# Kernel optimization log

Measured on AMD Instinct MI355X. Metric: run time of the kernel, lower is better.

Reference implementation:

```python
import jax, jax.numpy as jnp
import numpy as np

K = 16          # patch_size
P2 = 256        # patch_size**2
D_PD = 512      # learned base dictionary atoms (D_out_lam_pd)
D_LAM = 112     # adaptive atoms from sdict, = 8*14 (D_out_lam)
DD = D_PD + D_LAM  # 624
T = 5
INDICE = 112
MIN_V, MAX_V = 0.0, 1.0


def _idx(H, W, k, stride):
    oh = (H - k) // stride + 1
    ow = (W - k) // stride + 1
    r = jnp.arange(k)[:, None] + stride * jnp.arange(oh)[None, :]  # [k, oh]
    c = jnp.arange(k)[:, None] + stride * jnp.arange(ow)[None, :]  # [k, ow]
    return r[:, None, :, None], c[None, :, None, :], oh, ow


def _unfold(x, k, stride):
    # torch.nn.Unfold: [N, C*k*k, L] with (C, kh, kw) channel order, row-major L
    N, C, H, W = x.shape
    r, c, oh, ow = _idx(H, W, k, stride)
    return x[:, :, r, c].reshape(N, C * k * k, oh * ow)


def _fold(p, H, W, k):
    # torch.nn.functional.fold (col2im) with stride 1, overlap-add
    N, ckk, L = p.shape
    r, c, oh, ow = _idx(H, W, k, 1)
    C = ckk // (k * k)
    out = jnp.zeros((N, C, H, W), p.dtype)
    return out.at[:, :, r, c].add(p.reshape(N, C, k, k, oh, ow))


def _mlp(x, ws):
    # Linear + clamp(min=0) chain, no relu after last layer (dropout = eval identity)
    for w, b in ws[:-1]:
        x = jnp.maximum(x @ w + b, 0.0)
    w, b = ws[-1]
    return x @ w + b


def _cbam(x, w1, w2, conv_w):
    # standard CBAM: channel attention (shared MLP on avg+max pool) then 7x7 spatial attention
    def mlp(v):
        return jnp.maximum(v @ w1, 0.0) @ w2
    ca = jax.nn.sigmoid(mlp(x.mean(axis=(2, 3))) + mlp(x.max(axis=(2, 3))))
    x = x * ca[:, :, None, None]
    s = jnp.stack([x.mean(axis=1), x.max(axis=1)], axis=1)  # [N,2,h,w]
    sa = jax.lax.conv_general_dilated(s, conv_w, (1, 1), [(3, 3), (3, 3)],
                                      dimension_numbers=('NCHW', 'OIHW', 'NCHW'))
    return x * jax.nn.sigmoid(sa)


def _soft(x, l):
    return jnp.sign(x) * jnp.maximum(jnp.abs(x) - l, 0.0)


def _stage(img, Dict, c, sd_ws, ca1, ca2, saw, lam_ws, pd_ws, w_ws):
    N, C, H, W = img.shape
    uf = _unfold(img, K, 1).transpose(0, 2, 1)     # [N, L, 256]
    uf1 = _unfold(img, K, 8).transpose(0, 2, 1)    # [N, L1, 256]
    step = uf1.shape[1] // INDICE                  # static under jit
    ext = uf1[:, ::step, :][:, :INDICE, :]         # [N, 112, 256]
    sd = _mlp(ext, sd_ws)                          # linears1..4
    sd = sd / jnp.maximum(jnp.linalg.norm(sd, axis=-1, keepdims=True), 1e-12)
    sd = _cbam(sd.transpose(0, 2, 1).reshape(N, P2, 8, 14), ca1, ca2, saw)
    sd = sd.reshape(N, P2, INDICE)                 # [N, 256, 112]
    Dcat = jnp.concatenate([jnp.broadcast_to(Dict, (N,) + Dict.shape), sd], axis=-1)  # [N,256,624]
    # thresholds: l = cat(lpd, ls)
    thr = jnp.concatenate([_mlp(uf, pd_ws) / c, _mlp(uf, lam_ws) / c], axis=-1)  # [N,L,624]
    y = uf @ Dcat                                  # [N, L, 624]
    # S = (I - D^T D / c)^T; D^T D is symmetric so the transpose is a no-op
    S = jnp.eye(DD, dtype=img.dtype) - (Dcat.transpose(0, 2, 1) @ Dcat) / c
    z = _soft(y, thr)
    for _ in range(T):  # LISTA unrolled iterations (T static)
        z = _soft(z @ S + y / c, thr)
    Wg = jax.nn.sigmoid(_mlp(uf, w_ws))            # [N, L, 256]
    x_pred = jnp.clip(z @ Dcat.transpose(0, 2, 1), MIN_V, MAX_V) * Wg
    num = _fold(x_pred.transpose(0, 2, 1), H, W, K)
    den = _fold(Wg.transpose(0, 2, 1), H, W, K)    # fold of W * ones
    return num / den


def _forward(x, Dict, c, s1w, s1b, s2w, s2b, s3w, s3b, s4w, s4b, caw1, caw2, saw,
             a1w, a1b, a2w, a2b, a3w, a3b, p1w, p1b, p2w, p2b, p3w, p3b,
             b1w, b1b, b2w, b2b, b3w, b3b, q1w, q1b, q2w, q2b, q3w, q3b,
             w1w, w1b, w2w, w2b, w3w, w3b):
    sd_ws = [(s1w, s1b), (s2w, s2b), (s3w, s3b), (s4w, s4b)]
    w_ws = [(w1w, w1b), (w2w, w2b), (w3w, w3b)]
    res = _stage(x, Dict, c, sd_ws, caw1, caw2, saw,
                 [(a1w, a1b), (a2w, a2b), (a3w, a3b)],
                 [(p1w, p1b), (p2w, p2b), (p3w, p3b)], w_ws)
    res = _stage(res, Dict, c, sd_ws, caw1, caw2, saw,
                 [(b1w, b1b), (b2w, b2b), (b3w, b3b)],
                 [(q1w, q1b), (q2w, q2b), (q3w, q3b)], w_ws)
    return res


def setup_inputs() -> dict:
    key = jax.random.key(0)
    ks = iter(jax.random.split(key, 40))
    d = {}
    d['x'] = jax.random.uniform(next(ks), (2, 1, 128, 128), jnp.float32)
    Dm = jax.random.normal(next(ks), (P2, D_PD), jnp.float32)
    d['Dict'] = Dm / jnp.linalg.norm(Dm, axis=0, keepdims=True)  # unit-norm atoms
    d['c'] = jnp.asarray(10.0, jnp.float32)  # c > ||D^T D||_2
    dims = {'s1': (256, 512), 's2': (512, 1024), 's3': (1024, 512), 's4': (512, 256),
            'a1': (256, 1024), 'a2': (1024, 512), 'a3': (512, 112),
            'p1': (256, 1024), 'p2': (1024, 512), 'p3': (512, 512),
            'b1': (256, 1024), 'b2': (1024, 512), 'b3': (512, 112),
            'q1': (256, 1024), 'q2': (1024, 512), 'q3': (512, 512),
            'w1': (256, 1024), 'w2': (1024, 512), 'w3': (512, 256)}
    for name, (i, o) in dims.items():
        d[name + 'w'] = jax.random.normal(next(ks), (i, o), jnp.float32) / np.float32(np.sqrt(i))
        d[name + 'b'] = jnp.zeros((o,), jnp.float32)
    d['caw1'] = jax.random.normal(next(ks), (256, 512), jnp.float32) / np.float32(16.0)
    d['caw2'] = jax.random.normal(next(ks), (512, 256), jnp.float32) / np.float32(np.sqrt(512))
    d['saw'] = jax.random.normal(next(ks), (1, 2, 7, 7), jnp.float32) * np.float32(0.1)
    return d


def reference(x, Dict, c, s1w, s1b, s2w, s2b, s3w, s3b, s4w, s4b, caw1, caw2, saw,
              a1w, a1b, a2w, a2b, a3w, a3b, p1w, p1b, p2w, p2b, p3w, p3b,
              b1w, b1b, b2w, b2b, b3w, b3b, q1w, q1b, q2w, q2b, q3w, q3b,
              w1w, w1b, w2w, w2b, w3w, w3b):
    return _forward(x, Dict, c, s1w, s1b, s2w, s2b, s3w, s3b, s4w, s4b, caw1, caw2, saw,
                    a1w, a1b, a2w, a2b, a3w, a3b, p1w, p1b, p2w, p2b, p3w, p3b,
                    b1w, b1b, b2w, b2b, b3w, b3b, q1w, q1b, q2w, q2b, q3w, q3b,
                    w1w, w1b, w2w, w2b, w3w, w3b)
```

## Files before the change

kernel.cpp:

```cpp
#include <hip/hip_runtime.h>
#include <hip/hip_bf16.h>
#include <math.h>

#define L_LOC 12769
#define NB 2
#define NLR (NB * L_LOC)
#define NW 19

typedef short short8v __attribute__((ext_vector_type(8)));
typedef float f32x4 __attribute__((ext_vector_type(4)));
typedef __hip_bfloat16 bf16;

__device__ __forceinline__ float softf(float x, float l) {
  float a = fmaxf(fabsf(x) - l, 0.0f);
  return x > 0.0f ? a : (x < 0.0f ? -a : 0.0f);
}
__device__ __forceinline__ float sigf(float x) { return 1.0f / (1.0f + expf(-x)); }
__device__ __forceinline__ void split2(float v, bf16& h, bf16& l) {
  h = __float2bfloat16(v);
  l = __float2bfloat16(v - __bfloat162float(h));
}

enum { ME_RELU = 0, ME_SCALE = 1, ME_SIG = 2, ME_Y = 3, ME_SOFT = 4, ME_XP = 5,
       ME_SMAT = 6, ME_LIN = 7 };

template <int EPI, int TERMS, int WLO>
__global__ __launch_bounds__(256) void mgemm_k(
    const bf16* __restrict__ A, int lda, size_t aOff,
    const bf16* __restrict__ B0, const bf16* __restrict__ B1, int ldb, size_t bOff,
    void* __restrict__ Cv, int ldc, size_t cOff,
    bf16* __restrict__ Zp,
    const float* __restrict__ bias,
    const float* __restrict__ E1, const float* __restrict__ E2, int lde,
    const float* __restrict__ cptr, int bRow, int Rc, int r0, int N, int K)
{
  const int NPA = (TERMS >= 3) ? 2 : 1;
  const int NPB = (TERMS >= 2) ? 2 : 1;
  __shared__ char As[(TERMS >= 3) ? 2 : 1][8192];
  __shared__ char Bs[(TERMS >= 2) ? 2 : 1][8192];
  const int t = threadIdx.x;
  const int lane = t & 63, wv = t >> 6;
  const int wr = wv >> 1, wc = wv & 1;
  const int m0 = blockIdx.x * 128, n0 = blockIdx.y * 128;
  const int nb = (m0 >= bRow) ? 1 : 0;
  const bf16* __restrict__ Bt = nb ? B1 : B0;
  const int row16 = lane & 15, kg = lane >> 4;
  const int grow = t >> 2;
  const int gcol = (t & 3) * 8;
  f32x4 acc[4][4];
#pragma unroll
  for (int i = 0; i < 4; ++i)
#pragma unroll
    for (int j = 0; j < 4; ++j) { acc[i][j][0] = 0.f; acc[i][j][1] = 0.f; acc[i][j][2] = 0.f; acc[i][j][3] = 0.f; }

  for (int k0 = 0; k0 < K; k0 += 32) {
#pragma unroll
    for (int h = 0; h < NPA; ++h)
#pragma unroll
      for (int i = 0; i < 2; ++i) {
        const bf16* ga = A + h * aOff + (size_t)(m0 + i * 64 + grow) * lda + k0 + gcol;
        __builtin_amdgcn_global_load_lds(
            (const __attribute__((address_space(1))) void*)ga,
            (__attribute__((address_space(3))) void*)(As[h] + i * 4096 + wv * 1024), 16, 0, 0);
      }
#pragma unroll
    for (int h = 0; h < NPB; ++h)
#pragma unroll
      for (int i = 0; i < 2; ++i) {
        const bf16* gb = Bt + h * bOff + (size_t)(n0 + i * 64 + grow) * ldb + k0 + gcol;
        __builtin_amdgcn_global_load_lds(
            (const __attribute__((address_space(1))) void*)gb,
            (__attribute__((address_space(3))) void*)(Bs[h] + i * 4096 + wv * 1024), 16, 0, 0);
      }
    __syncthreads();
    short8v ah[4], al[4], bh[4], bl[4];
#pragma unroll
    for (int mi = 0; mi < 4; ++mi) {
      int o = (wr * 64 + mi * 16 + row16) * 64 + kg * 16;
      ah[mi] = *(const short8v*)(As[0] + o);
      if (TERMS >= 3) al[mi] = *(const short8v*)(As[NPA - 1] + o);
    }
#pragma unroll
    for (int ni = 0; ni < 4; ++ni) {
      int o = (wc * 64 + ni * 16 + row16) * 64 + kg * 16;
      bh[ni] = *(const short8v*)(Bs[0] + o);
      if (TERMS >= 2) bl[ni] = *(const short8v*)(Bs[NPB - 1] + o);
    }
#pragma unroll
    for (int mi = 0; mi < 4; ++mi)
#pragma unroll
      for (int ni = 0; ni < 4; ++ni) {
        if (TERMS >= 2)
          acc[mi][ni] = __builtin_amdgcn_mfma_f32_16x16x32_bf16(ah[mi], bl[ni], acc[mi][ni], 0, 0, 0);
        if (TERMS >= 3)
          acc[mi][ni] = __builtin_amdgcn_mfma_f32_16x16x32_bf16(al[mi], bh[ni], acc[mi][ni], 0, 0, 0);
        acc[mi][ni] = __builtin_amdgcn_mfma_f32_16x16x32_bf16(ah[mi], bh[ni], acc[mi][ni], 0, 0, 0);
      }
    __syncthreads();
  }

  float invc = 1.0f;
  if (EPI == ME_SCALE || EPI == ME_SOFT || EPI == ME_SMAT) invc = 1.0f / cptr[0];
  bf16* Cb = (bf16*)Cv;
  float* Cf = (float*)Cv;
#pragma unroll
  for (int ni = 0; ni < 4; ++ni) {
    int col = n0 + wc * 64 + ni * 16 + row16;
    const bool colok = col < N;
    float bv = 0.0f;
    if ((EPI == ME_RELU || EPI == ME_SCALE || EPI == ME_SIG || EPI == ME_LIN) && colok)
      bv = bias[col];
#pragma unroll
    for (int mi = 0; mi < 4; ++mi) {
      int rowb = m0 + wr * 64 + mi * 16 + kg * 4;
#pragma unroll
      for (int r = 0; r < 4; ++r) {
        int row = rowb + r;
        float v = acc[mi][ni][r];
        if (EPI == ME_RELU) {
          if (colok) {
            float o = fmaxf(v + bv, 0.0f);
            size_t ci = (size_t)row * ldc + col;
            if (WLO) {
              bf16 h, l; split2(o, h, l);
              Cb[ci] = h; Cb[ci + cOff] = l;
            } else {
              Cb[ci] = __float2bfloat16(o);
            }
          }
        } else if (EPI == ME_LIN) {
          if (colok && row < Rc) Cf[(size_t)row * ldc + col] = v + bv;
        } else if (EPI == ME_SCALE) {
          if (colok) Cf[(size_t)row * ldc + col] = (v + bv) * invc;
        } else if (EPI == ME_SIG) {
          if (colok) {
            int rl = row - nb * bRow;
            if (rl < Rc && rl >= 0)
              Cf[(size_t)col * NLR + (size_t)nb * L_LOC + r0 + rl] = sigf(v + bv);
          }
        } else if (EPI == ME_Y) {
          if (colok) {
            size_t e = (size_t)row * lde + col;
            Cf[(size_t)row * ldc + col] = v;
            Zp[(size_t)row * 640 + col] = __float2bfloat16(softf(v, E1[e]));
          }
        } else if (EPI == ME_SOFT) {
          if (colok) {
            size_t e = (size_t)row * lde + col;
            Cb[(size_t)row * ldc + col] = __float2bfloat16(softf(v + E1[e] * invc, E2[e]));
          }
        } else if (EPI == ME_XP) {
          int rl = row - nb * bRow;
          if (colok && rl < Rc && rl >= 0) {
            size_t g = (size_t)col * NLR + (size_t)nb * L_LOC + r0 + rl;
            Cf[g] = fminf(fmaxf(v, 0.0f), 1.0f) * E1[g];
          }
        } else {
          float o = (row < 624 && col < 624) ? ((row == col ? 1.0f : 0.0f) - v * invc) : 0.0f;
          bf16 h, l; split2(o, h, l);
          size_t ci = (size_t)row * ldc + col;
          Cb[ci] = h; Cb[ci + cOff] = l;
        }
      }
    }
  }
}

static void mgemm(hipStream_t st, int EPI, int terms, int wlo,
                  const bf16* A, int lda, size_t aOff,
                  const bf16* B0, const bf16* B1, int ldb, size_t bOff,
                  void* C, int ldc, size_t cOff,
                  bf16* Zp,
                  const float* bias, const float* E1, const float* E2, int lde,
                  const float* cptr, int bRow, int Rc, int r0,
                  int Mp, int N, int K)
{
  dim3 grid(Mp / 128, (N + 127) / 128), blk(256);
#define MG(ep, tm, wl) mgemm_k<ep, tm, wl><<<grid, blk, 0, st>>>(A, lda, aOff, B0, B1, ldb, bOff, C, ldc, cOff, Zp, bias, E1, E2, lde, cptr, bRow, Rc, r0, N, K)
  if (EPI == ME_RELU && terms == 1 && !wlo) { MG(ME_RELU, 1, 0); }
  else if (EPI == ME_RELU && terms == 1)    { MG(ME_RELU, 1, 1); }
  else if (EPI == ME_RELU)                  { MG(ME_RELU, 3, 1); }
  else if (EPI == ME_LIN)                   { MG(ME_LIN, 3, 0); }
  else if (EPI == ME_SCALE)                 { MG(ME_SCALE, 3, 0); }
  else if (EPI == ME_SIG)                   { MG(ME_SIG, 1, 0); }
  else if (EPI == ME_Y)                     { MG(ME_Y, 3, 0); }
  else if (EPI == ME_SOFT)                  { MG(ME_SOFT, 2, 0); }
  else if (EPI == ME_XP)                    { MG(ME_XP, 2, 0); }
  else                                      { MG(ME_SMAT, 3, 0); }
#undef MG
}

struct WTable {
  const float* src[NW];
  bf16* dst[NW];
  int K[NW], N[NW], Kp[NW], Np[NW];
  long long loOff[NW];
  int base[NW + 1];
};

__global__ void wtransall_k(WTable w) {
  int idx = blockIdx.x * 256 + threadIdx.x;
  if (idx >= w.base[NW]) return;
  int s = 0;
  while (s < NW - 1 && idx >= w.base[s + 1]) ++s;
  int li = idx - w.base[s];
  int Kp = w.Kp[s];
  int n = li / Kp, k = li - n * Kp;
  float v = (n < w.N[s] && k < w.K[s]) ? w.src[s][(size_t)k * w.N[s] + n] : 0.0f;
  bf16 h, l; split2(v, h, l);
  w.dst[s][li] = h;
  w.dst[s][li + w.loOff[s]] = l;
}

__global__ void extb_k(const float* __restrict__ img, bf16* __restrict__ dst) {
  int idx = blockIdx.x * 256 + threadIdx.x;
  int row = idx >> 8, p = idx & 255;
  float v = 0.0f;
  if (row < 224) {
    int n = row / 112, e = row - n * 112;
    int l1 = 2 * e, i1 = l1 / 15, j1 = l1 - i1 * 15;
    v = img[n * 16384 + (8 * i1 + (p >> 4)) * 128 + 8 * j1 + (p & 15)];
  }
  bf16 h, l; split2(v, h, l);
  dst[idx] = h; dst[idx + 65536] = l;
}

__global__ void rownorm224_k(float* sd) {
  int r = blockIdx.x, t = threadIdx.x;
  float v[4], s = 0.0f;
#pragma unroll
  for (int j = 0; j < 4; ++j) { v[j] = sd[r * 256 + t + 64 * j]; s += v[j] * v[j]; }
#pragma unroll
  for (int o = 1; o < 64; o <<= 1) s += __shfl_xor(s, o);
  float sc = 1.0f / fmaxf(sqrtf(s), 1e-12f);
#pragma unroll
  for (int j = 0; j < 4; ++j) sd[r * 256 + t + 64 * j] = v[j] * sc;
}

__global__ void meanmax_k(const float* __restrict__ sd, float* mv, float* xv) {
  int id = blockIdx.x * 256 + threadIdx.x;
  int n = id >> 8, ch = id & 255;
  float s = 0.0f, m = -INFINITY;
  for (int e = 0; e < 112; ++e) {
    float v = sd[(n * 112 + e) * 256 + ch];
    s += v; m = fmaxf(m, v);
  }
  mv[id] = s * (1.0f / 112.0f);
  xv[id] = m;
}

__global__ void cah_k(const float* __restrict__ mv, const float* __restrict__ xv,
                      const float* __restrict__ w1, float* hm, float* hx) {
  int id = blockIdx.x * 256 + threadIdx.x;
  int n = id >> 9, o = id & 511;
  float sm = 0.0f, sx = 0.0f;
#pragma unroll 4
  for (int i = 0; i < 256; ++i) {
    float w = w1[i * 512 + o];
    sm = fmaf(mv[n * 256 + i], w, sm);
    sx = fmaf(xv[n * 256 + i], w, sx);
  }
  hm[id] = fmaxf(sm, 0.0f);
  hx[id] = fmaxf(sx, 0.0f);
}

__global__ void cao_k(const float* __restrict__ hm, const float* __restrict__ hx,
                      const float* __restrict__ w2, float* ca) {
  int id = blockIdx.x * 256 + threadIdx.x;
  int n = id >> 8, ch = id & 255;
  float s = 0.0f;
#pragma unroll 4
  for (int o = 0; o < 512; ++o)
    s = fmaf(hm[n * 512 + o] + hx[n * 512 + o], w2[o * 256 + ch], s);
  ca[id] = sigf(s);
}

__global__ void spatial_k(const float* __restrict__ sd, const float* __restrict__ ca,
                          const float* __restrict__ saw, float* __restrict__ Dcat) {
  __shared__ float smean[112], smax[112];
  const int n = blockIdx.x, t = threadIdx.x;
  if (t < 112) {
    float sum = 0.0f, mx = -INFINITY;
    for (int ch = 0; ch < 256; ++ch) {
      float v = sd[(n * 112 + t) * 256 + ch] * ca[n * 256 + ch];
      Dcat[(size_t)n * 159744 + ch * 624 + 512 + t] = v;
      sum += v; mx = fmaxf(mx, v);
    }
    smean[t] = sum * (1.0f / 256.0f);
    smax[t] = mx;
  }
  __syncthreads();
  if (t < 112) {
    int h = t / 14, w = t % 14;
    float acc = 0.0f;
    for (int dh = 0; dh < 7; ++dh) {
      int hh = h + dh - 3; if (hh < 0 || hh >= 8) continue;
      for (int dw = 0; dw < 7; ++dw) {
        int ww = w + dw - 3; if (ww < 0 || ww >= 14) continue;
        int sp = hh * 14 + ww;
        acc += smean[sp] * saw[dh * 7 + dw] + smax[sp] * saw[49 + dh * 7 + dw];
      }
    }
    float sg = sigf(acc);
    for (int ch = 0; ch < 256; ++ch) Dcat[(size_t)n * 159744 + ch * 624 + 512 + t] *= sg;
  }
}

__global__ void dcatconv_k(const float* __restrict__ Dict, const float* __restrict__ Dc,
                           bf16* __restrict__ Db, bf16* __restrict__ DbT) {
  int idx = blockIdx.x * 256 + threadIdx.x;
  if (idx >= 327680) return;
  int n = idx / 163840, r = idx - n * 163840;
  int p = r / 640, a = r - p * 640;
  float v = 0.0f;
  if (a < 512)      v = Dict[p * 512 + a];
  else if (a < 624) v = Dc[(size_t)n * 159744 + p * 624 + a];
  bf16 h, l; split2(v, h, l);
  size_t base = (size_t)n * 327680;
  Db[base + p * 640 + a] = h;
  Db[base + 163840 + p * 640 + a] = l;
  DbT[base + (size_t)a * 256 + p] = h;
  DbT[base + 163840 + (size_t)a * 256 + p] = l;
}

__global__ void unfold_k(const float* __restrict__ img, bf16* __restrict__ uf,
                         int r0, int Rc, int bRowc, size_t pOff) {
  int bi = blockIdx.x;
  int nb = bi >= Rc;
  int rl = nb ? bi - Rc : bi;
  int row = nb * bRowc + rl;
  int p = threadIdx.x;
  int l = r0 + rl;
  int i0 = l / 113, j0 = l - i0 * 113;
  float v = img[nb * 16384 + (i0 + (p >> 4)) * 128 + j0 + (p & 15)];
  bf16 h, lo; split2(v, h, lo);
  size_t o = (size_t)row * 256 + p;
  uf[o] = h; uf[o + pOff] = lo;
}

__global__ void folddiv_k(const float* __restrict__ xpT, const float* __restrict__ wgT,
                          float* __restrict__ out) {
  int idx = blockIdx.x * 256 + threadIdx.x;
  if (idx >= 32768) return;
  int n = idx >> 14, rem = idx & 16383;
  int i = rem >> 7, j = rem & 127;
  float num = 0.0f, den = 0.0f;
  int kh0 = (i - 112 > 0) ? i - 112 : 0;
  int kh1 = (i < 15) ? i : 15;
  int kw0 = (j - 112 > 0) ? j - 112 : 0;
  int kw1 = (j < 15) ? j : 15;
  for (int kh = kh0; kh <= kh1; ++kh)
    for (int kw = kw0; kw <= kw1; ++kw) {
      int l = (i - kh) * 113 + (j - kw);
      size_t base = (size_t)(kh * 16 + kw) * NLR + (size_t)n * L_LOC + l;
      num += xpT[base];
      den += wgT[base];
    }
  out[idx] = num / den;
}

struct Bufs {
  float *xp, *wg, *Dcat_f, *sd, *res;
  float *mv, *xv, *hm, *hx, *ca;
  bf16 *Db, *DbT, *Sb;
  bf16 *extb, *sdh1, *sdh2, *sdh3;
  bf16 *uf, *h1, *h2, *z, *zn;
  float *thr, *y;
  size_t ufO, h2O;
  int R;
};

static void run_stage(hipStream_t st, const float* const* in, const float* img,
                      float* outimg, int pd0, int lam0,
                      bf16* const* WtPd, bf16* const* WtLam, bf16* const* WtW,
                      bf16* const* Ws, const Bufs& b)
{
  const float* cptr = in[2];
  const int BIG = 1 << 30;
  extb_k<<<dim3(256), dim3(256), 0, st>>>(img, b.extb);
  mgemm(st, ME_RELU, 3, 1, b.extb, 256, 65536, Ws[0], Ws[0], 256, 512 * 256,
        b.sdh1, 512, 256 * 512, 0, in[4], 0, 0, 0, cptr, BIG, 224, 0, 256, 512, 256);
  mgemm(st, ME_RELU, 3, 1, b.sdh1, 512, 256 * 512, Ws[1], Ws[1], 512, 1024 * 512,
        b.sdh2, 1024, 256 * 1024, 0, in[6], 0, 0, 0, cptr, BIG, 224, 0, 256, 1024, 512);
  mgemm(st, ME_RELU, 3, 1, b.sdh2, 1024, 256 * 1024, Ws[2], Ws[2], 1024, 512 * 1024,
        b.sdh3, 512, 256 * 512, 0, in[8], 0, 0, 0, cptr, BIG, 224, 0, 256, 512, 1024);
  mgemm(st, ME_LIN, 3, 0, b.sdh3, 512, 256 * 512, Ws[3], Ws[3], 512, 256 * 512,
        b.sd, 256, 0, 0, in[10], 0, 0, 0, cptr, BIG, 224, 0, 256, 256, 512);
  rownorm224_k<<<dim3(224), dim3(64), 0, st>>>(b.sd);
  meanmax_k<<<dim3(2), dim3(256), 0, st>>>(b.sd, b.mv, b.xv);
  cah_k<<<dim3(4), dim3(256), 0, st>>>(b.mv, b.xv, in[41], b.hm, b.hx);
  cao_k<<<dim3(2), dim3(256), 0, st>>>(b.hm, b.hx, in[42], b.ca);
  spatial_k<<<dim3(2), dim3(128), 0, st>>>(b.sd, b.ca, in[43], b.Dcat_f);
  dcatconv_k<<<dim3(1280), dim3(256), 0, st>>>(in[1], b.Dcat_f, b.Db, b.DbT);
  for (int n = 0; n < NB; ++n) {
    const bf16* Dt = b.DbT + (size_t)n * 327680;
    mgemm(st, ME_SMAT, 3, 0, Dt, 256, 163840, Dt, Dt, 256, 163840,
          b.Sb + (size_t)n * 819200, 640, 409600, 0,
          0, 0, 0, 0, cptr, BIG, 624, 0, 640, 640, 256);
  }

  for (int r0 = 0; r0 < L_LOC; r0 += b.R) {
    int Rc = L_LOC - r0; if (Rc > b.R) Rc = b.R;
    int bRowc = ((Rc + 127) / 128) * 128;
    int Mp = 2 * bRowc;
    unfold_k<<<dim3(2 * Rc), dim3(256), 0, st>>>(img, b.uf, r0, Rc, bRowc, b.ufO);
    mgemm(st, ME_RELU, 1, 0, b.uf, 256, b.ufO, WtPd[0], WtPd[0], 256, 1024 * 256,
          b.h1, 1024, 0, 0, in[pd0 + 1], 0, 0, 0, cptr, bRowc, Rc, r0, Mp, 1024, 256);
    mgemm(st, ME_RELU, 1, 1, b.h1, 1024, 0, WtPd[1], WtPd[1], 1024, 512 * 1024,
          b.h2, 512, b.h2O, 0, in[pd0 + 3], 0, 0, 0, cptr, bRowc, Rc, r0, Mp, 512, 1024);
    mgemm(st, ME_SCALE, 3, 0, b.h2, 512, b.h2O, WtPd[2], WtPd[2], 512, 512 * 512,
          b.thr, 640, 0, 0, in[pd0 + 5], 0, 0, 0, cptr, bRowc, Rc, r0, Mp, 512, 512);
    mgemm(st, ME_RELU, 1, 0, b.uf, 256, b.ufO, WtLam[0], WtLam[0], 256, 1024 * 256,
          b.h1, 1024, 0, 0, in[lam0 + 1], 0, 0, 0, cptr, bRowc, Rc, r0, Mp, 1024, 256);
    mgemm(st, ME_RELU, 1, 1, b.h1, 1024, 0, WtLam[1], WtLam[1], 1024, 512 * 1024,
          b.h2, 512, b.h2O, 0, in[lam0 + 3], 0, 0, 0, cptr, bRowc, Rc, r0, Mp, 512, 1024);
    mgemm(st, ME_SCALE, 3, 0, b.h2, 512, b.h2O, WtLam[2], WtLam[2], 512, 128 * 512,
          b.thr + 512, 640, 0, 0, in[lam0 + 5], 0, 0, 0, cptr, bRowc, Rc, r0, Mp, 112, 512);
    mgemm(st, ME_RELU, 1, 0, b.uf, 256, b.ufO, WtW[0], WtW[0], 256, 1024 * 256,
          b.h1, 1024, 0, 0, in[36], 0, 0, 0, cptr, bRowc, Rc, r0, Mp, 1024, 256);
    mgemm(st, ME_RELU, 1, 1, b.h1, 1024, 0, WtW[1], WtW[1], 1024, 512 * 1024,
          b.h2, 512, b.h2O, 0, in[38], 0, 0, 0, cptr, bRowc, Rc, r0, Mp, 512, 1024);
    mgemm(st, ME_SIG, 1, 0, b.h2, 512, b.h2O, WtW[2], WtW[2], 512, 256 * 512,
          b.wg, 0, 0, 0, in[40], 0, 0, 0, cptr, bRowc, Rc, r0, Mp, 256, 512);
    mgemm(st, ME_Y, 3, 0, b.uf, 256, b.ufO, b.DbT, b.DbT + 327680, 256, 163840,
          b.y, 640, 0, b.z, 0, b.thr, 0, 640, cptr, bRowc, Rc, r0, Mp, 624, 256);
    bf16* zi = b.z; bf16* zo = b.zn;
    for (int it = 0; it < 5; ++it) {
      mgemm(st, ME_SOFT, 2, 0, zi, 640, 0, b.Sb, b.Sb + 819200, 640, 409600,
            zo, 640, 0, 0, 0, b.y, b.thr, 640, cptr, bRowc, Rc, r0, Mp, 624, 640);
      bf16* tmp = zi; zi = zo; zo = tmp;
    }
    mgemm(st, ME_XP, 2, 0, zi, 640, 0, b.Db, b.Db + 327680, 640, 163840,
          b.xp, 0, 0, 0, 0, b.wg, 0, 0, cptr, bRowc, Rc, r0, Mp, 256, 640);
  }
  folddiv_k<<<dim3(128), dim3(256), 0, st>>>(b.xp, b.wg, outimg);
}

extern "C" void kernel_launch(void* const* d_in, const int* in_sizes, int n_in,
                              void* d_out, int out_size, void* d_ws, size_t ws_size,
                              hipStream_t stream)
{
  (void)in_sizes; (void)n_in; (void)out_size;
  const float* const* in = (const float* const*)d_in;
  char* base = (char*)d_ws;
  size_t off = 0;
  auto allocf = [&](size_t nelem) -> float* {
    float* p = (float*)(base + off);
    off += ((nelem * 4 + 255) / 256) * 256;
    return p;
  };
  auto allocb2 = [&](size_t nelem) -> bf16* {
    bf16* p = (bf16*)(base + off);
    off += ((nelem * 2 * 2 + 255) / 256) * 256;
    return p;
  };
  auto allocb1 = [&](size_t nelem) -> bf16* {
    bf16* p = (bf16*)(base + off);
    off += ((nelem * 2 + 255) / 256) * 256;
    return p;
  };
  Bufs b;
  b.xp = allocf((size_t)NLR * 256);
  b.wg = allocf((size_t)NLR * 256);
  b.Dcat_f = allocf(2 * 256 * 624);
  b.sd = allocf(224 * 256);
  b.res = allocf(2 * 16384);
  b.mv = allocf(512); b.xv = allocf(512);
  b.hm = allocf(1024); b.hx = allocf(1024);
  b.ca = allocf(512);
  b.Db = allocb2(2 * 163840);
  b.DbT = allocb2(2 * 163840);
  b.Sb = allocb2(2 * 409600);
  b.extb = allocb2(256 * 256);
  b.sdh1 = allocb2(256 * 512);
  b.sdh2 = allocb2(256 * 1024);
  b.sdh3 = allocb2(256 * 512);

  bf16 *Wa[3], *Wp[3], *Wb[3], *Wq[3], *Ww[3], *Ws[4];
  WTable wt;
  int ne = 0, tot = 0;
  auto addw = [&](const float* src, bf16* dst, int K, int N, int Kp, int Np) {
    wt.src[ne] = src; wt.dst[ne] = dst;
    wt.K[ne] = K; wt.N[ne] = N; wt.Kp[ne] = Kp; wt.Np[ne] = Np;
    wt.loOff[ne] = (long long)Np * Kp; wt.base[ne] = tot;
    tot += Np * Kp; ++ne;
  };
  int sdK[4] = {256, 512, 1024, 512}, sdN[4] = {512, 1024, 512, 256}, sdIdx[4] = {3, 5, 7, 9};
  for (int i = 0; i < 4; ++i) {
    Ws[i] = allocb2((size_t)sdN[i] * sdK[i]);
    addw(in[sdIdx[i]], Ws[i], sdK[i], sdN[i], sdK[i], sdN[i]);
  }
  struct WD { bf16** slot; int idx, K, N, Kp, Np; };
  WD wd[15] = {
    {&Wa[0], 11, 256, 1024, 256, 1024}, {&Wa[1], 13, 1024, 512, 1024, 512}, {&Wa[2], 15, 512, 112, 512, 128},
    {&Wp[0], 17, 256, 1024, 256, 1024}, {&Wp[1], 19, 1024, 512, 1024, 512}, {&Wp[2], 21, 512, 512, 512, 512},
    {&Wb[0], 23, 256, 1024, 256, 1024}, {&Wb[1], 25, 1024, 512, 1024, 512}, {&Wb[2], 27, 512, 112, 512, 128},
    {&Wq[0], 29, 256, 1024, 256, 1024}, {&Wq[1], 31, 1024, 512, 1024, 512}, {&Wq[2], 33, 512, 512, 512, 512},
    {&Ww[0], 35, 256, 1024, 256, 1024}, {&Ww[1], 37, 1024, 512, 1024, 512}, {&Ww[2], 39, 512, 256, 512, 256},
  };
  for (int i = 0; i < 15; ++i) {
    *wd[i].slot = allocb2((size_t)wd[i].Np * wd[i].Kp);
    addw(in[wd[i].idx], *wd[i].slot, wd[i].K, wd[i].N, wd[i].Kp, wd[i].Np);
  }
  wt.base[NW] = tot;
  wtransall_k<<<dim3((tot + 255) / 256), dim3(256), 0, stream>>>(wt);

  long long avail = (long long)ws_size - (long long)off - (1 << 20);
  long long perrow2 = 2LL * (12800 + 64);
  int R = 12800;
  if (avail / perrow2 < 12800) R = (int)(avail / perrow2);
  R &= ~127;
  if (R < 128) R = 128;
  b.R = R;
  size_t rows2 = (size_t)2 * R;
  b.uf = allocb2(rows2 * 256);  b.ufO = rows2 * 256;
  b.h1 = allocb1(rows2 * 1024);
  b.h2 = allocb2(rows2 * 512);  b.h2O = rows2 * 512;
  b.z = allocb1(rows2 * 640);
  b.zn = allocb1(rows2 * 640);
  b.thr = allocf(rows2 * 640);
  b.y = allocf(rows2 * 640);

  run_stage(stream, in, in[0], b.res, 17, 11, Wp, Wa, Ww, Ws, b);
  run_stage(stream, in, b.res, (float*)d_out, 29, 23, Wq, Wb, Ww, Ws, b);
}
```

Baseline: 3.189 ms.

## Split S-matrix diagonal out in fp32 to cut ISTA GEMM to one term; parallelize fold

Takes the diagonal of the S matrix (I - D^T D / c) out into a separate fp32 vector and zeroes it in the bf16 hi/lo split. The ISTA soft-threshold GEMM then runs with one bf16 term instead of two, and the diagonal contribution is added exactly in the epilogue by reading z back. The fold/divide kernel now spreads each pixel's kernel-row loop over 8 threads and combines them with a shuffle reduction, giving 8x more threads. The risk is lost precision from dropping the low-order term on the off-diagonal S entries, plus an extra read of z in the epilogue.

```diff
diff --git a/kernel.cpp b/kernel.cpp
--- a/kernel.cpp
+++ b/kernel.cpp
@@ -29,7 +29,7 @@
     const bf16* __restrict__ A, int lda, size_t aOff,
     const bf16* __restrict__ B0, const bf16* __restrict__ B1, int ldb, size_t bOff,
     void* __restrict__ Cv, int ldc, size_t cOff,
-    bf16* __restrict__ Zp,
+    bf16* __restrict__ Zp, float* __restrict__ Dg,
     const float* __restrict__ bias,
     const float* __restrict__ E1, const float* __restrict__ E2, int lde,
     const float* __restrict__ cptr, int bRow, int Rc, int r0, int N, int K)
@@ -110,6 +110,8 @@
     float bv = 0.0f;
     if ((EPI == ME_RELU || EPI == ME_SCALE || EPI == ME_SIG || EPI == ME_LIN) && colok)
       bv = bias[col];
+    float dgv = 0.0f;
+    if (EPI == ME_SOFT && colok) dgv = Dg[nb * 640 + col];
 #pragma unroll
     for (int mi = 0; mi < 4; ++mi) {
       int rowb = m0 + wr * 64 + mi * 16 + kg * 4;
@@ -147,7 +149,9 @@
         } else if (EPI == ME_SOFT) {
           if (colok) {
             size_t e = (size_t)row * lde + col;
-            Cb[(size_t)row * ldc + col] = __float2bfloat16(softf(v + E1[e] * invc, E2[e]));
+            float zin = __bfloat162float(Zp[(size_t)row * 640 + col]);
+            float v2 = v + zin * dgv + E1[e] * invc;
+            Cb[(size_t)row * ldc + col] = __float2bfloat16(softf(v2, E2[e]));
           }
         } else if (EPI == ME_XP) {
           int rl = row - nb * bRow;
@@ -157,6 +161,7 @@
           }
         } else {
           float o = (row < 624 && col < 624) ? ((row == col ? 1.0f : 0.0f) - v * invc) : 0.0f;
+          if (row == col && row < 624) { Dg[col] = o; o = 0.0f; }
           bf16 h, l; split2(o, h, l);
           size_t ci = (size_t)row * ldc + col;
           Cb[ci] = h; Cb[ci + cOff] = l;
@@ -170,13 +175,13 @@
                   const bf16* A, int lda, size_t aOff,
                   const bf16* B0, const bf16* B1, int ldb, size_t bOff,
                   void* C, int ldc, size_t cOff,
-                  bf16* Zp,
+                  bf16* Zp, float* Dg,
                   const float* bias, const float* E1, const float* E2, int lde,
                   const float* cptr, int bRow, int Rc, int r0,
                   int Mp, int N, int K)
 {
   dim3 grid(Mp / 128, (N + 127) / 128), blk(256);
-#define MG(ep, tm, wl) mgemm_k<ep, tm, wl><<<grid, blk, 0, st>>>(A, lda, aOff, B0, B1, ldb, bOff, C, ldc, cOff, Zp, bias, E1, E2, lde, cptr, bRow, Rc, r0, N, K)
+#define MG(ep, tm, wl) mgemm_k<ep, tm, wl><<<grid, blk, 0, st>>>(A, lda, aOff, B0, B1, ldb, bOff, C, ldc, cOff, Zp, Dg, bias, E1, E2, lde, cptr, bRow, Rc, r0, N, K)
   if (EPI == ME_RELU && terms == 1 && !wlo) { MG(ME_RELU, 1, 0); }
   else if (EPI == ME_RELU && terms == 1)    { MG(ME_RELU, 1, 1); }
   else if (EPI == ME_RELU)                  { MG(ME_RELU, 3, 1); }
@@ -184,7 +189,7 @@
   else if (EPI == ME_SCALE)                 { MG(ME_SCALE, 3, 0); }
   else if (EPI == ME_SIG)                   { MG(ME_SIG, 1, 0); }
   else if (EPI == ME_Y)                     { MG(ME_Y, 3, 0); }
-  else if (EPI == ME_SOFT)                  { MG(ME_SOFT, 2, 0); }
+  else if (EPI == ME_SOFT)                  { MG(ME_SOFT, 1, 0); }
   else if (EPI == ME_XP)                    { MG(ME_XP, 2, 0); }
   else                                      { MG(ME_SMAT, 3, 0); }
 #undef MG
@@ -341,27 +346,34 @@
 __global__ void folddiv_k(const float* __restrict__ xpT, const float* __restrict__ wgT,
                           float* __restrict__ out) {
   int idx = blockIdx.x * 256 + threadIdx.x;
-  if (idx >= 32768) return;
-  int n = idx >> 14, rem = idx & 16383;
+  if (idx >= 262144) return;
+  int g = idx & 7;
+  int pix = idx >> 3;
+  int n = pix >> 14, rem = pix & 16383;
   int i = rem >> 7, j = rem & 127;
   float num = 0.0f, den = 0.0f;
   int kh0 = (i - 112 > 0) ? i - 112 : 0;
   int kh1 = (i < 15) ? i : 15;
   int kw0 = (j - 112 > 0) ? j - 112 : 0;
   int kw1 = (j < 15) ? j : 15;
-  for (int kh = kh0; kh <= kh1; ++kh)
+  for (int kh = kh0 + ((g - kh0) & 7); kh <= kh1; kh += 8)
     for (int kw = kw0; kw <= kw1; ++kw) {
       int l = (i - kh) * 113 + (j - kw);
       size_t base = (size_t)(kh * 16 + kw) * NLR + (size_t)n * L_LOC + l;
       num += xpT[base];
       den += wgT[base];
     }
-  out[idx] = num / den;
+#pragma unroll
+  for (int o = 1; o < 8; o <<= 1) {
+    num += __shfl_xor(num, o);
+    den += __shfl_xor(den, o);
+  }
+  if (g == 0) out[pix] = num / den;
 }
 
 struct Bufs {
   float *xp, *wg, *Dcat_f, *sd, *res;
-  float *mv, *xv, *hm, *hx, *ca;
+  float *mv, *xv, *hm, *hx, *ca, *Dg;
   bf16 *Db, *DbT, *Sb;
   bf16 *extb, *sdh1, *sdh2, *sdh3;
   bf16 *uf, *h1, *h2, *z, *zn;
@@ -379,13 +391,13 @@
   const int BIG = 1 << 30;
   extb_k<<<dim3(256), dim3(256), 0, st>>>(img, b.extb);
   mgemm(st, ME_RELU, 3, 1, b.extb, 256, 65536, Ws[0], Ws[0], 256, 512 * 256,
-        b.sdh1, 512, 256 * 512, 0, in[4], 0, 0, 0, cptr, BIG, 224, 0, 256, 512, 256);
+        b.sdh1, 512, 256 * 512, 0, 0, in[4], 0, 0, 0, cptr, BIG, 224, 0, 256, 512, 256);
   mgemm(st, ME_RELU, 3, 1, b.sdh1, 512, 256 * 512, Ws[1], Ws[1], 512, 1024 * 512,
-        b.sdh2, 1024, 256 * 1024, 0, in[6], 0, 0, 0, cptr, BIG, 224, 0, 256, 1024, 512);
+        b.sdh2, 1024, 256 * 1024, 0, 0, in[6], 0, 0, 0, cptr, BIG, 224, 0, 256, 1024, 512);
   mgemm(st, ME_RELU, 3, 1, b.sdh2, 1024, 256 * 1024, Ws[2], Ws[2], 1024, 512 * 1024,
-        b.sdh3, 512, 256 * 512, 0, in[8], 0, 0, 0, cptr, BIG, 224, 0, 256, 512, 1024);
+        b.sdh3, 512, 256 * 512, 0, 0, in[8], 0, 0, 0, cptr, BIG, 224, 0, 256, 512, 1024);
   mgemm(st, ME_LIN, 3, 0, b.sdh3, 512, 256 * 512, Ws[3], Ws[3], 512, 256 * 512,
-        b.sd, 256, 0, 0, in[10], 0, 0, 0, cptr, BIG, 224, 0, 256, 256, 512);
+        b.sd, 256, 0, 0, 0, in[10], 0, 0, 0, cptr, BIG, 224, 0, 256, 256, 512);
   rownorm224_k<<<dim3(224), dim3(64), 0, st>>>(b.sd);
   meanmax_k<<<dim3(2), dim3(256), 0, st>>>(b.sd, b.mv, b.xv);
   cah_k<<<dim3(4), dim3(256), 0, st>>>(b.mv, b.xv, in[41], b.hm, b.hx);
@@ -395,7 +407,7 @@
   for (int n = 0; n < NB; ++n) {
     const bf16* Dt = b.DbT + (size_t)n * 327680;
     mgemm(st, ME_SMAT, 3, 0, Dt, 256, 163840, Dt, Dt, 256, 163840,
-          b.Sb + (size_t)n * 819200, 640, 409600, 0,
+          b.Sb + (size_t)n * 819200, 640, 409600, 0, b.Dg + n * 640,
           0, 0, 0, 0, cptr, BIG, 624, 0, 640, 640, 256);
   }
 
@@ -405,35 +417,35 @@
     int Mp = 2 * bRowc;
     unfold_k<<<dim3(2 * Rc), dim3(256), 0, st>>>(img, b.uf, r0, Rc, bRowc, b.ufO);
     mgemm(st, ME_RELU, 1, 0, b.uf, 256, b.ufO, WtPd[0], WtPd[0], 256, 1024 * 256,
-          b.h1, 1024, 0, 0, in[pd0 + 1], 0, 0, 0, cptr, bRowc, Rc, r0, Mp, 1024, 256);
+          b.h1, 1024, 0, 0, 0, in[pd0 + 1], 0, 0, 0, cptr, bRowc, Rc, r0, Mp, 1024, 256);
     mgemm(st, ME_RELU, 1, 1, b.h1, 1024, 0, WtPd[1], WtPd[1], 1024, 512 * 1024,
-          b.h2, 512, b.h2O, 0, in[pd0 + 3], 0, 0, 0, cptr, bRowc, Rc, r0, Mp, 512, 1024);
+          b.h2, 512, b.h2O, 0, 0, in[pd0 + 3], 0, 0, 0, cptr, bRowc, Rc, r0, Mp, 512, 1024);
     mgemm(st, ME_SCALE, 3, 0, b.h2, 512, b.h2O, WtPd[2], WtPd[2], 512, 512 * 512,
-          b.thr, 640, 0, 0, in[pd0 + 5], 0, 0, 0, cptr, bRowc, Rc, r0, Mp, 512, 512);
+          b.thr, 640, 0, 0, 0, in[pd0 + 5], 0, 0, 0, cptr, bRowc, Rc, r0, Mp, 512, 512);
     mgemm(st, ME_RELU, 1, 0, b.uf, 256, b.ufO, WtLam[0], WtLam[0], 256, 1024 * 256,
-          b.h1, 1024, 0, 0, in[lam0 + 1], 0, 0, 0, cptr, bRowc, Rc, r0, Mp, 1024, 256);
+          b.h1, 1024, 0, 0, 0, in[lam0 + 1], 0, 0, 0, cptr, bRowc, Rc, r0, Mp, 1024, 256);
     mgemm(st, ME_RELU, 1, 1, b.h1, 1024, 0, WtLam[1], WtLam[1], 1024, 512 * 1024,
-          b.h2, 512, b.h2O, 0, in[lam0 + 3], 0, 0, 0, cptr, bRowc, Rc, r0, Mp, 512, 1024);
+          b.h2, 512, b.h2O, 0, 0, in[lam0 + 3], 0, 0, 0, cptr, bRowc, Rc, r0, Mp, 512, 1024);
     mgemm(st, ME_SCALE, 3, 0, b.h2, 512, b.h2O, WtLam[2], WtLam[2], 512, 128 * 512,
-          b.thr + 512, 640, 0, 0, in[lam0 + 5], 0, 0, 0, cptr, bRowc, Rc, r0, Mp, 112, 512);
+          b.thr + 512, 640, 0, 0, 0, in[lam0 + 5], 0, 0, 0, cptr, bRowc, Rc, r0, Mp, 112, 512);
     mgemm(st, ME_RELU, 1, 0, b.uf, 256, b.ufO, WtW[0], WtW[0], 256, 1024 * 256,
-          b.h1, 1024, 0, 0, in[36], 0, 0, 0, cptr, bRowc, Rc, r0, Mp, 1024, 256);
+          b.h1, 1024, 0, 0, 0, in[36], 0, 0, 0, cptr, bRowc, Rc, r0, Mp, 1024, 256);
     mgemm(st, ME_RELU, 1, 1, b.h1, 1024, 0, WtW[1], WtW[1], 1024, 512 * 1024,
-          b.h2, 512, b.h2O, 0, in[38], 0, 0, 0, cptr, bRowc, Rc, r0, Mp, 512, 1024);
+          b.h2, 512, b.h2O, 0, 0, in[38], 0, 0, 0, cptr, bRowc, Rc, r0, Mp, 512, 1024);
     mgemm(st, ME_SIG, 1, 0, b.h2, 512, b.h2O, WtW[2], WtW[2], 512, 256 * 512,
-          b.wg, 0, 0, 0, in[40], 0, 0, 0, cptr, bRowc, Rc, r0, Mp, 256, 512);
+          b.wg, 0, 0, 0, 0, in[40], 0, 0, 0, cptr, bRowc, Rc, r0, Mp, 256, 512);
     mgemm(st, ME_Y, 3, 0, b.uf, 256, b.ufO, b.DbT, b.DbT + 327680, 256, 163840,
-          b.y, 640, 0, b.z, 0, b.thr, 0, 640, cptr, bRowc, Rc, r0, Mp, 624, 256);
+          b.y, 640, 0, b.z, 0, 0, b.thr, 0, 640, cptr, bRowc, Rc, r0, Mp, 624, 256);
     bf16* zi = b.z; bf16* zo = b.zn;
     for (int it = 0; it < 5; ++it) {
-      mgemm(st, ME_SOFT, 2, 0, zi, 640, 0, b.Sb, b.Sb + 819200, 640, 409600,
-            zo, 640, 0, 0, 0, b.y, b.thr, 640, cptr, bRowc, Rc, r0, Mp, 624, 640);
+      mgemm(st, ME_SOFT, 1, 0, zi, 640, 0, b.Sb, b.Sb + 819200, 640, 409600,
+            zo, 640, 0, zi, b.Dg, 0, b.y, b.thr, 640, cptr, bRowc, Rc, r0, Mp, 624, 640);
       bf16* tmp = zi; zi = zo; zo = tmp;
     }
     mgemm(st, ME_XP, 2, 0, zi, 640, 0, b.Db, b.Db + 327680, 640, 163840,
-          b.xp, 0, 0, 0, 0, b.wg, 0, 0, cptr, bRowc, Rc, r0, Mp, 256, 640);
-  }
-  folddiv_k<<<dim3(128), dim3(256), 0, st>>>(b.xp, b.wg, outimg);
+          b.xp, 0, 0, 0, 0, 0, b.wg, 0, 0, cptr, bRowc, Rc, r0, Mp, 256, 640);
+  }
+  folddiv_k<<<dim3(1024), dim3(256), 0, st>>>(b.xp, b.wg, outimg);
 }
 
 extern "C" void kernel_launch(void* const* d_in, const int* in_sizes, int n_in,
@@ -468,6 +480,7 @@
   b.mv = allocf(512); b.xv = allocf(512);
   b.hm = allocf(1024); b.hx = allocf(1024);
   b.ca = allocf(512);
+  b.Dg = allocf(2 * 640);
   b.Db = allocb2(2 * 163840);
   b.DbT = allocb2(2 * 163840);
   b.Sb = allocb2(2 * 409600);
```

Measured after the change: 3.144 ms. No clear change (-1.4%).
